# Kernel optimization log

Measured on AMD Instinct MI355X. Metric: run time of the kernel, lower is better.

Reference implementation:

```python
import jax, jax.numpy as jnp
import numpy as np

H_DIM = 64
GRID = 8
NS = 2.0  # neighborhood_size
S = 256   # number of sequences (scenes)
P = 64    # pedestrians per sequence
EPS = 1e-5


def setup_inputs() -> dict:
    key = jax.random.key(0)
    k = jax.random.split(key, 6)
    N = S * P
    G = GRID * GRID
    h_states = jax.random.normal(k[0], (1, N, H_DIM), jnp.float32)
    end_pos = jax.random.normal(k[1], (N, 2), jnp.float32)
    starts = (jnp.arange(S, dtype=jnp.int32) * P)
    seq_start_end = jnp.stack([starts, starts + P], axis=1)  # (S, 2)
    # mlp_pool: Linear(G*H_DIM -> H_DIM) + BatchNorm1d + ReLU
    W = jax.random.normal(k[2], (G * H_DIM, H_DIM), jnp.float32) / np.sqrt(G * H_DIM)
    b = jnp.zeros((H_DIM,), jnp.float32)
    gamma = jnp.ones((H_DIM,), jnp.float32)
    beta = jnp.zeros((H_DIM,), jnp.float32)
    return {"h_states": h_states, "seq_start_end": seq_start_end, "end_pos": end_pos,
            "W": W, "b": b, "gamma": gamma, "beta": beta}


def reference(h_states, seq_start_end, end_pos, W, b, gamma, beta):
    nseq = seq_start_end.shape[0]          # S (static)
    N = end_pos.shape[0]
    Hd = h_states.shape[-1]
    nped = N // nseq                       # P (static; equal-length sequences)
    G = GRID * GRID
    half = NS / 2.0

    h = h_states.reshape(N, Hd).reshape(nseq, nped, Hd)     # (S, P, H)
    pos = end_pos.reshape(nseq, nped, 2)                    # (S, P, 2)

    # bounds per center pedestrian i
    tl_x = pos[..., 0] - half   # (S, P)
    tl_y = pos[..., 1] + half
    br_x = pos[..., 0] + half
    br_y = pos[..., 1] - half

    # pairwise: axis 1 = center i, axis 2 = other k
    ox = pos[:, None, :, 0]     # (S, 1, P)
    oy = pos[:, None, :, 1]
    cell_x = jnp.floor((ox - tl_x[:, :, None]) / NS * GRID)
    cell_y = jnp.floor((tl_y[:, :, None] - oy) / NS * GRID)
    grid = cell_x + cell_y * GRID                            # (S, P, P)

    oob = ((ox >= br_x[:, :, None]) | (ox <= tl_x[:, :, None]) |
           (oy >= tl_y[:, :, None]) | (oy <= br_y[:, :, None]))
    diag = jnp.eye(nped, dtype=bool)[None]                   # self excluded (within_bound[0::P+1]=1)
    valid = (~oob) & (~diag)

    grid_i = jnp.clip(grid.astype(jnp.int32), 0, G - 1)      # masked entries don't matter
    seq_off = (jnp.arange(nseq, dtype=jnp.int32)[:, None, None] * nped
               + jnp.arange(nped, dtype=jnp.int32)[None, :, None]) * G
    dummy = nseq * nped * G
    ids = jnp.where(valid, seq_off + grid_i, dummy)          # (S, P, P)

    # data for (s, i, k) is hidden of other k (curr_hidden.repeat(num_ped, 1))
    data = jnp.broadcast_to(h[:, None, :, :], (nseq, nped, nped, Hd)).reshape(-1, Hd)
    pooled = jax.ops.segment_sum(data, ids.reshape(-1), num_segments=dummy + 1)[:-1]
    x = pooled.reshape(N, G * Hd)                            # (N, G*H), row i = concat over grid cells

    # mlp_pool: Linear -> BatchNorm1d (train mode, biased var) -> ReLU
    x = x @ W + b
    mu = jnp.mean(x, axis=0)
    var = jnp.mean((x - mu) ** 2, axis=0)
    x = gamma * (x - mu) / jnp.sqrt(var + EPS) + beta
    return jnp.maximum(x, 0.0)
```

## Files before the change

### kernel.cpp

```cpp
#include <hip/hip_runtime.h>
#include <hip/hip_bf16.h>


#define NSEQ 256
#define NTOT (NSEQ*64)
#define EPSV 1e-5f

typedef __attribute__((ext_vector_type(8))) short short8;
typedef __attribute__((ext_vector_type(4))) float f32x4;
typedef unsigned short ushort_t;

__device__ __forceinline__ ushort_t f2b(float f) {
    __hip_bfloat16 h = __float2bfloat16(f);
    return *reinterpret_cast<ushort_t*>(&h);
}
__device__ __forceinline__ int kperm(int k) {
    return ((k >> 5)*2 + ((k & 7) >> 2))*16 + ((k >> 3) & 3)*4 + (k & 3);
}

__global__ __launch_bounds__(256) void sp_transpose(
    const float* __restrict__ W, short* __restrict__ Wt, float* __restrict__ statbuf)
{
    __shared__ __align__(16) float Tl[64*68];
    const int b = blockIdx.x, tid = threadIdx.x;
    if (b == 0 && tid < 128) statbuf[tid] = 0.0f;
    const float* wg = W + (size_t)b*4096;
    for (int m = 0; m < 4; ++m) {
        int c = m*256 + tid;
        int k = c >> 4, t0 = (c & 15)*4;
        *(f32x4*)(Tl + k*68 + t0) = *(const f32x4*)(wg + k*64 + t0);
    }
    __syncthreads();
    for (int m = 0; m < 2; ++m) {
        int q = m*256 + tid;
        int col = q >> 3, k0 = (q & 7)*8;
        short8 o;
        #pragma unroll
        for (int i2 = 0; i2 < 8; ++i2)
            o[i2] = (short)f2b(Tl[kperm(k0 + i2)*68 + col]);
        *(short8*)(Wt + ((size_t)(b*64 + col)*64 + k0)) = o;
    }
}

#define SM_CM   9216
#define SM_POS  11264
#define SM_XS1  8704
#define SM_RED  17408
#define SM_TOT  19456

__global__ __launch_bounds__(512, 4) void sp_main(
    const float* __restrict__ h, const float* __restrict__ pos,
    const short* __restrict__ Wt, const float* __restrict__ bvec,
    float* __restrict__ X, float* __restrict__ statbuf)
{
    __shared__ __align__(16) char smem[SM_TOT];
    ushort_t*      Ht = (ushort_t*)(smem);
    unsigned char* cm = (unsigned char*)(smem + SM_CM);
    float*         px = (float*)(smem + SM_POS);
    float*         py = px + 64;

    const int b    = blockIdx.x;
    const int seq  = b >> 1;
    const int row0 = (b & 1) * 32;
    const int base = seq * 64;
    const int tid  = threadIdx.x;
    const int lane = tid & 63, w = tid >> 6;
    const int ln15 = lane & 15, ln4 = lane >> 4;
    const int xph  = (b >> 3) & 7;

    if (tid < 64) { px[tid] = pos[(base + tid)*2]; py[tid] = pos[(base + tid)*2 + 1]; }
    for (int m = 0; m < 2; ++m) {
        int c = m*512 + tid;
        int j = c >> 4, t0 = (c & 15)*4;
        f32x4 v = *(const f32x4*)(h + (size_t)(base + j)*64 + t0);
        #pragma unroll
        for (int u = 0; u < 4; ++u) Ht[(t0 + u)*72 + j] = f2b(v[u]);
    }
    __syncthreads();

    for (int m = 0; m < 4; ++m) {
        int p = m*512 + tid;
        int il = p >> 6, j = p & 63;
        int i  = row0 + il;
        unsigned char val = 255;
        if (i != j) {
            float ax = px[i], ay = py[i], ox = px[j], oy = py[j];
            float tlx = ax - 1.0f, tly = ay + 1.0f, brx = ax + 1.0f, bry = ay - 1.0f;
            bool oob = (ox >= brx) | (ox <= tlx) | (oy >= tly) | (oy <= bry);
            if (!oob) {
                int g = (int)(floorf((ox - tlx)*4.0f) + floorf((tly - oy)*4.0f)*8.0f);
                g = g < 0 ? 0 : (g > 63 ? 63 : g);
                val = (unsigned char)g;
            }
        }
        cm[il*64 + j] = val;
    }
    __syncthreads();

    short8 hf2[4][2];
    #pragma unroll
    for (int mt = 0; mt < 4; ++mt)
        #pragma unroll
        for (int kt2 = 0; kt2 < 2; ++kt2)
            hf2[mt][kt2] = *(const short8*)(Ht + (mt*16 + ln15)*72 + kt2*32 + ln4*8);

    unsigned ohw[2][2][2];
    {
        const unsigned w8 = (unsigned)(w * 8);
        #pragma unroll
        for (int rt = 0; rt < 2; ++rt)
            #pragma unroll
            for (int kt = 0; kt < 2; ++kt) {
                const unsigned* cp = (const unsigned*)(cm + (rt*16 + ln15)*64 + kt*32 + ln4*8);
                #pragma unroll
                for (int half = 0; half < 2; ++half) {
                    unsigned cw = cp[half], oh = 0u;
                    #pragma unroll
                    for (int u = 0; u < 4; ++u) {
                        unsigned d = ((cw >> (8*u)) & 255u) - w8;
                        if (d < 8u) oh |= (1u << d) << (8*u);
                    }
                    ohw[rt][kt][half] = oh;
                }
            }
    }

    f32x4 acc[2][4];
    #pragma unroll
    for (int rt = 0; rt < 2; ++rt)
        #pragma unroll
        for (int nt = 0; nt < 4; ++nt) acc[rt][nt] = (f32x4){0.f,0.f,0.f,0.f};

    for (int cc = 0; cc < 8; ++cc) {
        const int c2 = (cc + xph) & 7;
        const int g  = w*8 + c2;
        const short* wgp = Wt + (size_t)g*4096;
        short8 bw[2][4];
        #pragma unroll
        for (int kt = 0; kt < 2; ++kt)
            #pragma unroll
            for (int nt = 0; nt < 4; ++nt)
                bw[kt][nt] = *(const short8*)(wgp + (nt*16 + ln15)*64 + kt*32 + ln4*8);

        #pragma unroll
        for (int rt = 0; rt < 2; ++rt) {
            short8 sf[2];
            #pragma unroll
            for (int kt = 0; kt < 2; ++kt) {
                unsigned t0 = (ohw[rt][kt][0] >> c2) & 0x01010101u;
                unsigned t1 = (ohw[rt][kt][1] >> c2) & 0x01010101u;
                union { unsigned u[4]; short8 s; } sfu;
                sfu.u[0] = ((t0 & 1u)          | ((t0 << 8) & 0x10000u)) * 0x3F80u;
                sfu.u[1] = (((t0 >> 16) & 1u)  | ((t0 >> 8) & 0x10000u)) * 0x3F80u;
                sfu.u[2] = ((t1 & 1u)          | ((t1 << 8) & 0x10000u)) * 0x3F80u;
                sfu.u[3] = (((t1 >> 16) & 1u)  | ((t1 >> 8) & 0x10000u)) * 0x3F80u;
                sf[kt] = sfu.s;
            }
            f32x4 pt[4];
            #pragma unroll
            for (int mt = 0; mt < 4; ++mt) pt[mt] = (f32x4){0.f,0.f,0.f,0.f};
            #pragma unroll
            for (int kt2 = 0; kt2 < 2; ++kt2)
                #pragma unroll
                for (int mt = 0; mt < 4; ++mt)
                    pt[mt] = __builtin_amdgcn_mfma_f32_16x16x32_bf16(hf2[mt][kt2], sf[kt2], pt[mt], 0, 0, 0);
            #pragma unroll
            for (int kt = 0; kt < 2; ++kt) {
                short8 af;
                #pragma unroll
                for (int r = 0; r < 4; ++r) {
                    af[r]     = (short)f2b(pt[2*kt    ][r]);
                    af[4 + r] = (short)f2b(pt[2*kt + 1][r]);
                }
                #pragma unroll
                for (int nt = 0; nt < 4; ++nt)
                    acc[rt][nt] = __builtin_amdgcn_mfma_f32_16x16x32_bf16(af, bw[kt][nt], acc[rt][nt], 0, 0, 0);
            }
        }
    }
    __syncthreads();

    float* Xs0 = (float*)smem;
    float* Xs1 = (float*)(smem + SM_XS1);
    for (int step = 0; step < 4; ++step) {
        if ((w & 3) == step) {
            float* Xs = (w < 4) ? Xs0 : Xs1;
            #pragma unroll
            for (int rt = 0; rt < 2; ++rt)
                #pragma unroll
                for (int nt = 0; nt < 4; ++nt)
                    #pragma unroll
                    for (int r = 0; r < 4; ++r) {
                        int row = rt*16 + ln4*4 + r;
                        int col = nt*16 + ln15;
                        if (step == 0) Xs[row*68 + col]  = acc[rt][nt][r];
                        else           Xs[row*68 + col] += acc[rt][nt][r];
                    }
        }
        __syncthreads();
    }

    {
        const int lr = tid >> 4, c0 = (tid & 15)*4;
        float* xg = X + (size_t)(base + row0 + lr)*64 + c0;
        f32x4 v;
        #pragma unroll
        for (int u = 0; u < 4; ++u) {
            int o = lr*68 + c0 + u;
            v[u] = Xs0[o] + Xs1[o] + bvec[c0 + u];
        }
        *(f32x4*)xg = v;
    }

    {
        float* red1 = (float*)(smem + SM_RED);
        float* red2 = red1 + 256;
        if (tid < 256) {
            int col = tid & 63, rg = tid >> 6;
            float bc = bvec[col], s1 = 0.f, s2 = 0.f;
            for (int ii = 0; ii < 8; ++ii) {
                int o = (rg*8 + ii)*68 + col;
                float xv = Xs0[o] + Xs1[o] + bc;
                s1 += xv; s2 += xv*xv;
            }
            red1[rg*64 + col] = s1;
            red2[rg*64 + col] = s2;
        }
        __syncthreads();
        if (tid < 128) {
            int hs = tid >> 6, c2 = tid & 63;
            const float* r0 = hs ? red2 : red1;
            float v = r0[c2] + r0[64 + c2] + r0[128 + c2] + r0[192 + c2];
            atomicAdd(statbuf + tid, v);
        }
    }
}

__global__ __launch_bounds__(256) void sp_finish(
    float* __restrict__ X, const float* __restrict__ statbuf,
    const float* __restrict__ gamma, const float* __restrict__ beta)
{
    __shared__ float scale[64], shift[64];
    const int b = blockIdx.x, tid = threadIdx.x;

    if (tid < 64) {
        const float inv_n = 1.0f / (float)NTOT;
        float mu  = statbuf[tid]      * inv_n;
        float var = statbuf[64 + tid] * inv_n - mu*mu;
        float sc  = gamma[tid] / sqrtf(var + EPSV);
        scale[tid] = sc;
        shift[tid] = beta[tid] - mu*sc;
    }
    __syncthreads();
    #pragma unroll
    for (int q = 0; q < 4; ++q) {
        size_t idx4 = (size_t)b*1024 + q*256 + tid;
        f32x4 v = ((f32x4*)X)[idx4];
        int c0 = ((int)idx4*4) & 63;
        #pragma unroll
        for (int u = 0; u < 4; ++u)
            v[u] = fmaxf(v[u]*scale[c0 + u] + shift[c0 + u], 0.0f);
        ((f32x4*)X)[idx4] = v;
    }
}

extern "C" void kernel_launch(void* const* d_in, const int* in_sizes, int n_in,
                              void* d_out, int out_size, void* d_ws, size_t ws_size,
                              hipStream_t stream)
{
    const float* h     = (const float*)d_in[0];
    const float* pos   = (const float*)d_in[2];
    const float* W     = (const float*)d_in[3];
    const float* bvec  = (const float*)d_in[4];
    const float* gamma = (const float*)d_in[5];
    const float* beta  = (const float*)d_in[6];

    float* X       = (float*)d_out;
    short* Wt      = (short*)d_ws;
    float* statbuf = (float*)((char*)d_ws + 524288);

    sp_transpose<<<64,      256, 0, stream>>>(W, Wt, statbuf);
    sp_main     <<<NSEQ*2,  512, 0, stream>>>(h, pos, Wt, bvec, X, statbuf);
    sp_finish   <<<NSEQ,    256, 0, stream>>>(X, statbuf, gamma, beta);
}
```

Baseline: 118.1 us.

## Stage H fragments in shared memory and spread BN stat atomics over slots

The per-thread register array of H MFMA fragments is replaced by a compact fragment-ordered copy in LDS. One wave writes it and every wave reloads four fragments per k-step, which lowers register pressure at the cost of extra LDS reads. The batch-norm sum atomics are also spread across 16 slots indexed by block to reduce contention on one address, and the finish kernel sums the slots. The zeroing in the transpose kernel is widened to cover the larger stats buffer, which depends on that buffer being allocated large enough.

```diff
diff --git a/kernel.cpp b/kernel.cpp
--- a/kernel.cpp
+++ b/kernel.cpp
@@ -23,7 +23,10 @@
 {
     __shared__ __align__(16) float Tl[64*68];
     const int b = blockIdx.x, tid = threadIdx.x;
-    if (b == 0 && tid < 128) statbuf[tid] = 0.0f;
+    if (b == 0) {
+        #pragma unroll
+        for (int q = 0; q < 8; ++q) statbuf[q*256 + tid] = 0.0f;
+    }
     const float* wg = W + (size_t)b*4096;
     for (int m = 0; m < 4; ++m) {
         int c = m*256 + tid;
@@ -44,9 +47,10 @@
 
 #define SM_CM   9216
 #define SM_POS  11264
+#define SM_HF   11776
 #define SM_XS1  8704
 #define SM_RED  17408
-#define SM_TOT  19456
+#define SM_TOT  19968
 
 __global__ __launch_bounds__(512, 4) void sp_main(
     const float* __restrict__ h, const float* __restrict__ pos,
@@ -58,6 +62,7 @@
     unsigned char* cm = (unsigned char*)(smem + SM_CM);
     float*         px = (float*)(smem + SM_POS);
     float*         py = px + 64;
+    short*         Hf = (short*)(smem + SM_HF);
 
     const int b    = blockIdx.x;
     const int seq  = b >> 1;
@@ -95,14 +100,15 @@
         }
         cm[il*64 + j] = val;
     }
-    __syncthreads();
-
-    short8 hf2[4][2];
-    #pragma unroll
-    for (int mt = 0; mt < 4; ++mt)
-        #pragma unroll
-        for (int kt2 = 0; kt2 < 2; ++kt2)
-            hf2[mt][kt2] = *(const short8*)(Ht + (mt*16 + ln15)*72 + kt2*32 + ln4*8);
+    if (tid < 64) {
+        #pragma unroll
+        for (int f = 0; f < 8; ++f) {
+            int mt = f >> 1, kt2 = f & 1;
+            short8 v = *(const short8*)(Ht + (mt*16 + ln15)*72 + kt2*32 + ln4*8);
+            *(short8*)(Hf + (f*64 + lane)*8) = v;
+        }
+    }
+    __syncthreads();
 
     unsigned ohw[2][2][2];
     {
@@ -160,10 +166,15 @@
             #pragma unroll
             for (int mt = 0; mt < 4; ++mt) pt[mt] = (f32x4){0.f,0.f,0.f,0.f};
             #pragma unroll
-            for (int kt2 = 0; kt2 < 2; ++kt2)
+            for (int kt2 = 0; kt2 < 2; ++kt2) {
+                short8 hm[4];
                 #pragma unroll
                 for (int mt = 0; mt < 4; ++mt)
-                    pt[mt] = __builtin_amdgcn_mfma_f32_16x16x32_bf16(hf2[mt][kt2], sf[kt2], pt[mt], 0, 0, 0);
+                    hm[mt] = *(const short8*)(Hf + (((mt*2 + kt2)*64 + lane))*8);
+                #pragma unroll
+                for (int mt = 0; mt < 4; ++mt)
+                    pt[mt] = __builtin_amdgcn_mfma_f32_16x16x32_bf16(hm[mt], sf[kt2], pt[mt], 0, 0, 0);
+            }
             #pragma unroll
             for (int kt = 0; kt < 2; ++kt) {
                 short8 af;
@@ -231,7 +242,7 @@
             int hs = tid >> 6, c2 = tid & 63;
             const float* r0 = hs ? red2 : red1;
             float v = r0[c2] + r0[64 + c2] + r0[128 + c2] + r0[192 + c2];
-            atomicAdd(statbuf + tid, v);
+            atomicAdd(statbuf + (b & 15)*128 + tid, v);
         }
     }
 }
@@ -245,8 +256,14 @@
 
     if (tid < 64) {
         const float inv_n = 1.0f / (float)NTOT;
-        float mu  = statbuf[tid]      * inv_n;
-        float var = statbuf[64 + tid] * inv_n - mu*mu;
+        float s1 = 0.f, s2 = 0.f;
+        #pragma unroll
+        for (int s = 0; s < 16; ++s) {
+            s1 += statbuf[s*128 + tid];
+            s2 += statbuf[s*128 + 64 + tid];
+        }
+        float mu  = s1 * inv_n;
+        float var = s2 * inv_n - mu*mu;
         float sc  = gamma[tid] / sqrtf(var + EPSV);
         scale[tid] = sc;
         shift[tid] = beta[tid] - mu*sc;
```

Result: faster. 111.2 us (-5.8%).
